# Optimization experiments

Measured on AMD Instinct MI355X. Metric: run time of the kernel, lower is better.

## Reference

```python
import jax, jax.numpy as jnp
import numpy as np

H = 8          # num_heads
WIN = 63       # win_size
LEFT = WIN - 1 - WIN // 2  # 31
EPS = 1e-5


def layer_norm(x, w, b):
    mu = x.mean(-1, keepdims=True)
    var = ((x - mu) ** 2).mean(-1, keepdims=True)
    return (x - mu) / jnp.sqrt(var + EPS) * w + b


def setup_inputs() -> dict:
    key = jax.random.key(0)
    N, T, C = 2, 2048, 512
    hid = 4 * C
    ks = jax.random.split(key, 16)
    s = 0.02
    return {
        "x": jax.random.normal(ks[0], (N, T, C), jnp.float32),
        "norm1_w": jnp.ones((C,), jnp.float32),
        "norm1_b": jnp.zeros((C,), jnp.float32),
        "qkv_w": jax.random.normal(ks[1], (3 * C, C), jnp.float32) * s,
        "qkv_b": jnp.zeros((3 * C,), jnp.float32),
        "rel_bias": jax.random.normal(ks[2], (H, WIN), jnp.float32) * s,
        "proj_w": jax.random.normal(ks[3], (C, C), jnp.float32) * s,
        "proj_b": jnp.zeros((C,), jnp.float32),
        "norm2_w": jnp.ones((C,), jnp.float32),
        "norm2_b": jnp.zeros((C,), jnp.float32),
        "fc1_w": jax.random.normal(ks[4], (hid, C), jnp.float32) * s,
        "fc1_b": jnp.zeros((hid,), jnp.float32),
        "fc2_w": jax.random.normal(ks[5], (C, hid), jnp.float32) * s,
        "fc2_b": jnp.zeros((C,), jnp.float32),
    }


def reference(x, norm1_w, norm1_b, qkv_w, qkv_b, rel_bias, proj_w, proj_b,
              norm2_w, norm2_b, fc1_w, fc1_b, fc2_w, fc2_b):
    N, T, C = x.shape
    hd = C // H
    scale = hd ** -0.5
    right = WIN - LEFT - 1

    shortcut = x
    h = layer_norm(x, norm1_w, norm1_b)
    qkv = (h @ qkv_w.T + qkv_b).reshape(N, T, 3, H, hd)
    q, k, v = qkv[:, :, 0], qkv[:, :, 1], qkv[:, :, 2]  # (N,T,H,hd)

    # zero-pad keys/values along time, gather sliding windows
    kp = jnp.pad(k, ((0, 0), (LEFT, right), (0, 0), (0, 0)))
    vp = jnp.pad(v, ((0, 0), (LEFT, right), (0, 0), (0, 0)))
    idx = jnp.arange(T)[:, None] + jnp.arange(WIN)[None, :]
    k_win = kp[:, idx]
    v_win = vp[:, idx]

    attn = jnp.einsum('nthd,ntwhd->nhtw', q * scale, k_win)
    attn = attn + rel_bias[None, :, None, :]
    # boundary mask: key position j = t - LEFT + w must lie in [0, T)
    pos = idx - LEFT
    mask = jnp.where((pos < 0) | (pos >= T), jnp.float32(-100.0), jnp.float32(0.0))
    attn = attn + mask[None, None, :, :]
    attn = jax.nn.softmax(attn, axis=-1)

    out = jnp.einsum('nhtw,ntwhd->nthd', attn, v_win).reshape(N, T, C)
    out = out @ proj_w.T + proj_b

    x = shortcut + out
    h2 = layer_norm(x, norm2_w, norm2_b)
    m = jax.nn.gelu(h2 @ fc1_w.T + fc1_b, approximate=False)  # torch nn.GELU = exact erf
    m = m @ fc2_w.T + fc2_b
    return x + m
```

## Files before the change

kernel.cpp:

```cpp
#include <hip/hip_runtime.h>

typedef unsigned short u16;
typedef unsigned int uint;
typedef __attribute__((ext_vector_type(4))) float floatx4;
typedef __attribute__((ext_vector_type(16))) float floatx16;
typedef __attribute__((ext_vector_type(8))) short shortx8;

__device__ __forceinline__ u16 f2b(float f) {
    unsigned int u = __float_as_uint(f);
    unsigned int r = (u + 0x7fffu + ((u >> 16) & 1u)) >> 16;
    return (u16)r;
}
__device__ __forceinline__ float b2f(u16 u) {
    return __uint_as_float(((unsigned int)u) << 16);
}
__device__ __forceinline__ void gl_lds16(const u16* g, u16* l) {
    __builtin_amdgcn_global_load_lds(
        (const __attribute__((address_space(1))) void*)g,
        (__attribute__((address_space(3))) void*)l, 16, 0, 0);
}
__device__ __forceinline__ float gelu_f(float v) {
    float e = __expf(1.59576912f * v * (1.0f + 0.044715f * v * v));
    return v * e / (e + 1.0f);
}

__device__ __forceinline__ void ln_row(const float* __restrict__ x,
                                       const float* __restrict__ w,
                                       const float* __restrict__ b,
                                       u16* __restrict__ out, int row,
                                       float* red) {
    const float2* xr = (const float2*)(x + (size_t)row * 512);
    float2 v = xr[threadIdx.x];
    float s = v.x + v.y;
    float s2 = v.x * v.x + v.y * v.y;
    #pragma unroll
    for (int o = 32; o > 0; o >>= 1) {
        s += __shfl_down(s, o, 64);
        s2 += __shfl_down(s2, o, 64);
    }
    int wid = threadIdx.x >> 6, lane = threadIdx.x & 63;
    if (lane == 0) { red[wid] = s; red[4 + wid] = s2; }
    __syncthreads();
    s = red[0] + red[1] + red[2] + red[3];
    s2 = red[4] + red[5] + red[6] + red[7];
    float mu = s * (1.0f / 512.0f);
    float var = s2 * (1.0f / 512.0f) - mu * mu;
    float rstd = rsqrtf(var + 1e-5f);
    float2 wv = ((const float2*)w)[threadIdx.x];
    float2 bv = ((const float2*)b)[threadIdx.x];
    float o0 = (v.x - mu) * rstd * wv.x + bv.x;
    float o1 = (v.y - mu) * rstd * wv.y + bv.y;
    unsigned int pack = (unsigned)f2b(o0) | ((unsigned)f2b(o1) << 16);
    ((unsigned int*)(out + (size_t)row * 512))[threadIdx.x] = pack;
}

__global__ __launch_bounds__(256) void ln_kernel(const float* __restrict__ x,
                                                 const float* __restrict__ w,
                                                 const float* __restrict__ b,
                                                 u16* __restrict__ out) {
    __shared__ float red[8];
    ln_row(x, w, b, out, blockIdx.x, red);
}

__global__ __launch_bounds__(256) void prep_kernel(
    const float* __restrict__ qkvw, u16* __restrict__ wq,
    const float* __restrict__ projw, u16* __restrict__ wp,
    const float* __restrict__ fc1w, u16* __restrict__ w1,
    const float* __restrict__ fc2w, u16* __restrict__ w2,
    const float* __restrict__ x, const float* __restrict__ n1w,
    const float* __restrict__ n1b, u16* __restrict__ hb) {
    __shared__ float red[8];
    int bi = blockIdx.x;
    if (bi < 3072) {
        const float* src;
        u16* dst;
        int i0;
        if (bi < 768)       { src = qkvw; dst = wq; i0 = bi; }
        else if (bi < 1024) { src = projw; dst = wp; i0 = bi - 768; }
        else if (bi < 2048) { src = fc1w; dst = w1; i0 = bi - 1024; }
        else                { src = fc2w; dst = w2; i0 = bi - 2048; }
        int i = i0 * 256 + threadIdx.x;
        float4 v = ((const float4*)src)[i];
        uint2 o;
        o.x = (unsigned)f2b(v.x) | ((unsigned)f2b(v.y) << 16);
        o.y = (unsigned)f2b(v.z) | ((unsigned)f2b(v.w) << 16);
        ((uint2*)dst)[i] = o;
    } else {
        ln_row(x, n1w, n1b, hb, bi - 3072, red);
    }
}

template <int BM, int BN, int EPI>
__global__ __launch_bounds__(256) void gemm_lds(const u16* __restrict__ A,
                                                const u16* __restrict__ W,
                                                const float* __restrict__ bias,
                                                const float* __restrict__ resid,
                                                float* __restrict__ outF,
                                                u16* __restrict__ outB,
                                                int M, int Nn, int K) {
    constexpr int MI = BM / 2 / 32;
    constexpr int NI = BN / 2 / 32;
    __shared__ u16 a_s[BM * 64];
    __shared__ u16 b_s[BN * 64];

    int tid = threadIdx.x;
    int wid = tid >> 6, lane = tid & 63;
    int wm = wid >> 1, wn = wid & 1;
    int m_blk = blockIdx.y * BM;
    int n_blk = blockIdx.x * BN;
    int lr = lane & 31;
    int lk = lane >> 5;

    floatx16 acc[MI][NI];
    #pragma unroll
    for (int i = 0; i < MI; i++)
        #pragma unroll
        for (int j = 0; j < NI; j++)
            #pragma unroll
            for (int r = 0; r < 16; r++) acc[i][j][r] = 0.f;

    const u16* Ag = A + (size_t)m_blk * K;
    const u16* Wg = W + (size_t)n_blk * K;

    for (int k0 = 0; k0 < K; k0 += 64) {
        #pragma unroll
        for (int p = 0; p < BM * 8 / 256; p++) {
            int c = p * 256 + tid;
            int row = c >> 3;
            int kc = (c & 7) ^ (row & 7);
            gl_lds16(Ag + (size_t)row * K + k0 + kc * 8, a_s + c * 8);
        }
        #pragma unroll
        for (int p = 0; p < BN * 8 / 256; p++) {
            int c = p * 256 + tid;
            int row = c >> 3;
            int kc = (c & 7) ^ (row & 7);
            gl_lds16(Wg + (size_t)row * K + k0 + kc * 8, b_s + c * 8);
        }
        __syncthreads();
        #pragma unroll
        for (int s = 0; s < 4; s++) {
            shortx8 af[MI], bf[NI];
            int kc = s * 2 + lk;
            #pragma unroll
            for (int i = 0; i < MI; i++) {
                int row = wm * (BM / 2) + i * 32 + lr;
                af[i] = *(const shortx8*)(a_s + (row * 8 + (kc ^ (row & 7))) * 8);
            }
            #pragma unroll
            for (int j = 0; j < NI; j++) {
                int row = wn * (BN / 2) + j * 32 + lr;
                bf[j] = *(const shortx8*)(b_s + (row * 8 + (kc ^ (row & 7))) * 8);
            }
            #pragma unroll
            for (int i = 0; i < MI; i++)
                #pragma unroll
                for (int j = 0; j < NI; j++)
                    acc[i][j] = __builtin_amdgcn_mfma_f32_32x32x16_bf16(
                        af[i], bf[j], acc[i][j], 0, 0, 0);
        }
        __syncthreads();
    }

    int col_l = lane & 31;
    int row_q = 4 * (lane >> 5);
    #pragma unroll
    for (int nj = 0; nj < NI; nj++) {
        int col = n_blk + wn * (BN / 2) + nj * 32 + col_l;
        float bv = bias[col];
        #pragma unroll
        for (int mi = 0; mi < MI; mi++) {
            #pragma unroll
            for (int r = 0; r < 16; r++) {
                int row = m_blk + wm * (BM / 2) + mi * 32 + (r & 3) + 8 * (r >> 2) + row_q;
                size_t off = (size_t)row * Nn + col;
                float v = acc[mi][nj][r] + bv;
                if (EPI == 1 || EPI == 3) {
                    outF[off] = v + resid[off];
                } else if (EPI == 2) {
                    outB[off] = f2b(gelu_f(v));
                } else {
                    outB[off] = f2b(v);
                }
            }
        }
    }
}

__global__ __launch_bounds__(256) void attn_kernel(const u16* __restrict__ qkv,
                                                   const float* __restrict__ rel_bias,
                                                   u16* __restrict__ out) {
    __shared__ u16 k_s[128][72];
    __shared__ u16 v_t[64][152];
    __shared__ u16 p_s[4][16][104];
    __shared__ float s_bias[64];

    int bx = blockIdx.x;
    int n = bx >> 8;
    int h = (bx >> 5) & 7;
    int t0 = (bx & 31) << 6;
    int tid = threadIdx.x, wid = tid >> 6, lane = tid & 63;
    int col = lane & 15, rq = lane >> 4;

    const u16* qrow = qkv + (size_t)(n * 2048 + t0 + wid * 16 + col) * 1536 + h * 64 + rq * 8;
    shortx8 qf0 = *(const shortx8*)qrow;
    shortx8 qf1 = *(const shortx8*)(qrow + 32);

    if (tid < 63) s_bias[tid] = rel_bias[h * 63 + tid];
    if (tid == 63) s_bias[63] = 0.f;

    const uint* qkv_u = (const uint*)qkv;
    for (int idx = tid; idx < 128 * 32; idx += 256) {
        int row = idx >> 5, j = idx & 31;
        int pos = t0 - 31 + row;
        uint kv = 0;
        if (pos >= 0 && pos < 2048)
            kv = qkv_u[(size_t)(n * 2048 + pos) * 768 + 256 + h * 32 + j];
        *(uint*)&k_s[row][j * 2] = kv;
    }
    for (int idx = tid; idx < 144 * 32; idx += 256) {
        int row = idx >> 5, j = idx & 31;
        int pos = t0 - 31 + row;
        uint vv = 0;
        if (pos >= 0 && pos < 2048)
            vv = qkv_u[(size_t)(n * 2048 + pos) * 768 + 512 + h * 32 + j];
        v_t[2 * j][row] = (u16)(vv & 0xffffu);
        v_t[2 * j + 1][row] = (u16)(vv >> 16);
    }
    __syncthreads();

    floatx4 S[5];
    #pragma unroll
    for (int nt = 0; nt < 5; nt++) S[nt] = (floatx4){0.f, 0.f, 0.f, 0.f};
    #pragma unroll
    for (int nt = 0; nt < 5; nt++) {
        const u16* kb = &k_s[wid * 16 + nt * 16 + col][rq * 8];
        shortx8 b0 = *(const shortx8*)kb;
        shortx8 b1 = *(const shortx8*)(kb + 32);
        S[nt] = __builtin_amdgcn_mfma_f32_16x16x32_bf16(qf0, b0, S[nt], 0, 0, 0);
        S[nt] = __builtin_amdgcn_mfma_f32_16x16x32_bf16(qf1, b1, S[nt], 0, 0, 0);
    }

    #pragma unroll
    for (int r = 0; r < 4; r++) {
        int t_row = rq * 4 + r;
        float sc[5];
        float mx = -1e30f;
        #pragma unroll
        for (int nt = 0; nt < 5; nt++) {
            int w = nt * 16 + col - t_row;
            int pos_abs = t0 - 31 + wid * 16 + nt * 16 + col;
            float v;
            if (w < 0 || w > 62) {
                v = -1e30f;
            } else {
                v = S[nt][r] * 0.125f + s_bias[w];
                if (pos_abs < 0 || pos_abs >= 2048) v -= 100.f;
            }
            sc[nt] = v;
            mx = fmaxf(mx, v);
        }
        #pragma unroll
        for (int o = 1; o < 16; o <<= 1) mx = fmaxf(mx, __shfl_xor(mx, o, 64));
        float l = 0.f;
        #pragma unroll
        for (int nt = 0; nt < 5; nt++) {
            sc[nt] = __expf(sc[nt] - mx);
            l += sc[nt];
        }
        #pragma unroll
        for (int o = 1; o < 16; o <<= 1) l += __shfl_xor(l, o, 64);
        float inv = 1.0f / l;
        #pragma unroll
        for (int nt = 0; nt < 5; nt++)
            p_s[wid][t_row][nt * 16 + col] = f2b(sc[nt] * inv);
        p_s[wid][t_row][80 + col] = 0;
    }
    __syncthreads();

    floatx4 O[4];
    #pragma unroll
    for (int dt = 0; dt < 4; dt++) O[dt] = (floatx4){0.f, 0.f, 0.f, 0.f};
    const u16* pr = &p_s[wid][col][rq * 8];
    shortx8 a0 = *(const shortx8*)pr;
    shortx8 a1 = *(const shortx8*)(pr + 32);
    shortx8 a2 = *(const shortx8*)(pr + 64);
    #pragma unroll
    for (int dt = 0; dt < 4; dt++) {
        const u16* vb = &v_t[dt * 16 + col][wid * 16 + rq * 8];
        shortx8 b0 = *(const shortx8*)vb;
        shortx8 b1 = *(const shortx8*)(vb + 32);
        shortx8 b2 = *(const shortx8*)(vb + 64);
        O[dt] = __builtin_amdgcn_mfma_f32_16x16x32_bf16(a0, b0, O[dt], 0, 0, 0);
        O[dt] = __builtin_amdgcn_mfma_f32_16x16x32_bf16(a1, b1, O[dt], 0, 0, 0);
        O[dt] = __builtin_amdgcn_mfma_f32_16x16x32_bf16(a2, b2, O[dt], 0, 0, 0);
    }

    #pragma unroll
    for (int dt = 0; dt < 4; dt++) {
        #pragma unroll
        for (int r = 0; r < 4; r++) {
            int t_row = rq * 4 + r;
            out[(size_t)(n * 2048 + t0 + wid * 16 + t_row) * 512 + h * 64 + dt * 16 + col] =
                f2b(O[dt][r]);
        }
    }
}

extern "C" void kernel_launch(void* const* d_in, const int* in_sizes, int n_in,
                              void* d_out, int out_size, void* d_ws, size_t ws_size,
                              hipStream_t stream) {
    const float* x     = (const float*)d_in[0];
    const float* n1w   = (const float*)d_in[1];
    const float* n1b   = (const float*)d_in[2];
    const float* qkvw  = (const float*)d_in[3];
    const float* qkvbv = (const float*)d_in[4];
    const float* relb  = (const float*)d_in[5];
    const float* projw = (const float*)d_in[6];
    const float* projb = (const float*)d_in[7];
    const float* n2w   = (const float*)d_in[8];
    const float* n2b   = (const float*)d_in[9];
    const float* fc1w  = (const float*)d_in[10];
    const float* fc1b  = (const float*)d_in[11];
    const float* fc2w  = (const float*)d_in[12];
    const float* fc2b  = (const float*)d_in[13];
    float* out = (float*)d_out;

    char* p = (char*)d_ws;
    u16* wq   = (u16*)p;  p += (size_t)786432 * 2;
    u16* wp   = (u16*)p;  p += (size_t)262144 * 2;
    u16* w1   = (u16*)p;  p += (size_t)1048576 * 2;
    u16* w2   = (u16*)p;  p += (size_t)1048576 * 2;
    u16* hb   = (u16*)p;  p += (size_t)2097152 * 2;
    u16* qkvb = (u16*)p;  p += (size_t)6291456 * 2;
    u16* attb = (u16*)p;  p += (size_t)2097152 * 2;
    float* x2 = (float*)p; p += (size_t)2097152 * 4;
    u16* mb   = (u16*)p;  p += (size_t)8388608 * 2;

    prep_kernel<<<7168, 256, 0, stream>>>(qkvw, wq, projw, wp, fc1w, w1, fc2w, w2,
                                          x, n1w, n1b, hb);
    gemm_lds<128, 128, 0><<<dim3(12, 32), 256, 0, stream>>>(
        hb, wq, qkvbv, nullptr, nullptr, qkvb, 4096, 1536, 512);
    attn_kernel<<<512, 256, 0, stream>>>(qkvb, relb, attb);
    gemm_lds<128, 64, 1><<<dim3(8, 32), 256, 0, stream>>>(
        attb, wp, projb, x, x2, nullptr, 4096, 512, 512);
    ln_kernel<<<4096, 256, 0, stream>>>(x2, n2w, n2b, hb);
    gemm_lds<128, 128, 2><<<dim3(16, 32), 256, 0, stream>>>(
        hb, w1, fc1b, nullptr, nullptr, mb, 4096, 2048, 512);
    gemm_lds<128, 64, 3><<<dim3(8, 32), 256, 0, stream>>>(
        mb, w2, fc2b, x2, out, nullptr, 4096, 512, 2048);
}
```

Measured before the change: 195.3 us.

## Double-buffer GEMM LDS tiles, shrink tiles, and store residual x2 in bf16

Adds double-buffered LDS staging to the MFMA GEMM, so the next K-tile's global-to-LDS loads overlap with compute and one barrier per iteration is dropped. Tile sizes shrink for the QKV, proj, fc1 and fc2 GEMMs to launch more blocks, and launch_bounds asks for 3 blocks per CU. The intermediate residual x2 is stored as bf16 instead of fp32, and the second layernorm reads bf16, which cuts memory traffic. In exchange it doubles LDS use and loses some precision on the residual path.

```diff
diff --git a/kernel.cpp b/kernel.cpp
--- a/kernel.cpp
+++ b/kernel.cpp
@@ -54,12 +54,35 @@
     ((unsigned int*)(out + (size_t)row * 512))[threadIdx.x] = pack;
 }
 
-__global__ __launch_bounds__(256) void ln_kernel(const float* __restrict__ x,
-                                                 const float* __restrict__ w,
-                                                 const float* __restrict__ b,
-                                                 u16* __restrict__ out) {
+__global__ __launch_bounds__(256) void ln_kernel_b(const u16* __restrict__ x,
+                                                   const float* __restrict__ w,
+                                                   const float* __restrict__ b,
+                                                   u16* __restrict__ out) {
     __shared__ float red[8];
-    ln_row(x, w, b, out, blockIdx.x, red);
+    int row = blockIdx.x;
+    uint pv = ((const uint*)(x + (size_t)row * 512))[threadIdx.x];
+    float vx = b2f((u16)(pv & 0xffffu)), vy = b2f((u16)(pv >> 16));
+    float s = vx + vy;
+    float s2 = vx * vx + vy * vy;
+    #pragma unroll
+    for (int o = 32; o > 0; o >>= 1) {
+        s += __shfl_down(s, o, 64);
+        s2 += __shfl_down(s2, o, 64);
+    }
+    int wid = threadIdx.x >> 6, lane = threadIdx.x & 63;
+    if (lane == 0) { red[wid] = s; red[4 + wid] = s2; }
+    __syncthreads();
+    s = red[0] + red[1] + red[2] + red[3];
+    s2 = red[4] + red[5] + red[6] + red[7];
+    float mu = s * (1.0f / 512.0f);
+    float var = s2 * (1.0f / 512.0f) - mu * mu;
+    float rstd = rsqrtf(var + 1e-5f);
+    float2 wv = ((const float2*)w)[threadIdx.x];
+    float2 bv = ((const float2*)b)[threadIdx.x];
+    float o0 = (vx - mu) * rstd * wv.x + bv.x;
+    float o1 = (vy - mu) * rstd * wv.y + bv.y;
+    unsigned int pack = (unsigned)f2b(o0) | ((unsigned)f2b(o1) << 16);
+    ((unsigned int*)(out + (size_t)row * 512))[threadIdx.x] = pack;
 }
 
 __global__ __launch_bounds__(256) void prep_kernel(
@@ -91,17 +114,20 @@
 }
 
 template <int BM, int BN, int EPI>
-__global__ __launch_bounds__(256) void gemm_lds(const u16* __restrict__ A,
-                                                const u16* __restrict__ W,
-                                                const float* __restrict__ bias,
-                                                const float* __restrict__ resid,
-                                                float* __restrict__ outF,
-                                                u16* __restrict__ outB,
-                                                int M, int Nn, int K) {
+__global__ __launch_bounds__(256, 3) void gemm_lds(const u16* __restrict__ A,
+                                                   const u16* __restrict__ W,
+                                                   const float* __restrict__ bias,
+                                                   const float* __restrict__ residF,
+                                                   const u16* __restrict__ residB,
+                                                   float* __restrict__ outF,
+                                                   u16* __restrict__ outB,
+                                                   int M, int Nn, int K) {
     constexpr int MI = BM / 2 / 32;
     constexpr int NI = BN / 2 / 32;
-    __shared__ u16 a_s[BM * 64];
-    __shared__ u16 b_s[BN * 64];
+    constexpr int ACH = BM * 8 / 256;
+    constexpr int BCH = BN * 8 / 256;
+    __shared__ u16 a_s[2][BM * 64];
+    __shared__ u16 b_s[2][BN * 64];
 
     int tid = threadIdx.x;
     int wid = tid >> 6, lane = tid & 63;
@@ -122,22 +148,37 @@
     const u16* Ag = A + (size_t)m_blk * K;
     const u16* Wg = W + (size_t)n_blk * K;
 
-    for (int k0 = 0; k0 < K; k0 += 64) {
-        #pragma unroll
-        for (int p = 0; p < BM * 8 / 256; p++) {
-            int c = p * 256 + tid;
-            int row = c >> 3;
-            int kc = (c & 7) ^ (row & 7);
-            gl_lds16(Ag + (size_t)row * K + k0 + kc * 8, a_s + c * 8);
-        }
-        #pragma unroll
-        for (int p = 0; p < BN * 8 / 256; p++) {
-            int c = p * 256 + tid;
-            int row = c >> 3;
-            int kc = (c & 7) ^ (row & 7);
-            gl_lds16(Wg + (size_t)row * K + k0 + kc * 8, b_s + c * 8);
-        }
+    int arow[ACH], akc[ACH], brow[BCH], bkc[BCH];
+    #pragma unroll
+    for (int p = 0; p < ACH; p++) {
+        int c = p * 256 + tid;
+        arow[p] = c >> 3;
+        akc[p] = (c & 7) ^ (arow[p] & 7);
+    }
+    #pragma unroll
+    for (int p = 0; p < BCH; p++) {
+        int c = p * 256 + tid;
+        brow[p] = c >> 3;
+        bkc[p] = (c & 7) ^ (brow[p] & 7);
+    }
+
+    auto stage = [&](int k0, int buf) {
+        #pragma unroll
+        for (int p = 0; p < ACH; p++)
+            gl_lds16(Ag + (size_t)arow[p] * K + k0 + akc[p] * 8,
+                     a_s[buf] + (p * 256 + tid) * 8);
+        #pragma unroll
+        for (int p = 0; p < BCH; p++)
+            gl_lds16(Wg + (size_t)brow[p] * K + k0 + bkc[p] * 8,
+                     b_s[buf] + (p * 256 + tid) * 8);
+    };
+
+    stage(0, 0);
+    int nit = K >> 6;
+    for (int it = 0; it < nit; it++) {
         __syncthreads();
+        if (it + 1 < nit) stage((it + 1) << 6, (it + 1) & 1);
+        int cb = it & 1;
         #pragma unroll
         for (int s = 0; s < 4; s++) {
             shortx8 af[MI], bf[NI];
@@ -145,12 +186,12 @@
             #pragma unroll
             for (int i = 0; i < MI; i++) {
                 int row = wm * (BM / 2) + i * 32 + lr;
-                af[i] = *(const shortx8*)(a_s + (row * 8 + (kc ^ (row & 7))) * 8);
+                af[i] = *(const shortx8*)(a_s[cb] + (row * 8 + (kc ^ (row & 7))) * 8);
             }
             #pragma unroll
             for (int j = 0; j < NI; j++) {
                 int row = wn * (BN / 2) + j * 32 + lr;
-                bf[j] = *(const shortx8*)(b_s + (row * 8 + (kc ^ (row & 7))) * 8);
+                bf[j] = *(const shortx8*)(b_s[cb] + (row * 8 + (kc ^ (row & 7))) * 8);
             }
             #pragma unroll
             for (int i = 0; i < MI; i++)
@@ -159,7 +200,6 @@
                     acc[i][j] = __builtin_amdgcn_mfma_f32_32x32x16_bf16(
                         af[i], bf[j], acc[i][j], 0, 0, 0);
         }
-        __syncthreads();
     }
 
     int col_l = lane & 31;
@@ -175,10 +215,12 @@
                 int row = m_blk + wm * (BM / 2) + mi * 32 + (r & 3) + 8 * (r >> 2) + row_q;
                 size_t off = (size_t)row * Nn + col;
                 float v = acc[mi][nj][r] + bv;
-                if (EPI == 1 || EPI == 3) {
-                    outF[off] = v + resid[off];
+                if (EPI == 1) {
+                    outB[off] = f2b(v + residF[off]);
                 } else if (EPI == 2) {
                     outB[off] = f2b(gelu_f(v));
+                } else if (EPI == 3) {
+                    outF[off] = v + b2f(residB[off]);
                 } else {
                     outB[off] = f2b(v);
                 }
@@ -334,19 +376,19 @@
     u16* hb   = (u16*)p;  p += (size_t)2097152 * 2;
     u16* qkvb = (u16*)p;  p += (size_t)6291456 * 2;
     u16* attb = (u16*)p;  p += (size_t)2097152 * 2;
-    float* x2 = (float*)p; p += (size_t)2097152 * 4;
+    u16* x2b  = (u16*)p;  p += (size_t)2097152 * 2;
     u16* mb   = (u16*)p;  p += (size_t)8388608 * 2;
 
     prep_kernel<<<7168, 256, 0, stream>>>(qkvw, wq, projw, wp, fc1w, w1, fc2w, w2,
                                           x, n1w, n1b, hb);
-    gemm_lds<128, 128, 0><<<dim3(12, 32), 256, 0, stream>>>(
-        hb, wq, qkvbv, nullptr, nullptr, qkvb, 4096, 1536, 512);
+    gemm_lds<128, 64, 0><<<dim3(24, 32), 256, 0, stream>>>(
+        hb, wq, qkvbv, nullptr, nullptr, nullptr, qkvb, 4096, 1536, 512);
     attn_kernel<<<512, 256, 0, stream>>>(qkvb, relb, attb);
-    gemm_lds<128, 64, 1><<<dim3(8, 32), 256, 0, stream>>>(
-        attb, wp, projb, x, x2, nullptr, 4096, 512, 512);
-    ln_kernel<<<4096, 256, 0, stream>>>(x2, n2w, n2b, hb);
-    gemm_lds<128, 128, 2><<<dim3(16, 32), 256, 0, stream>>>(
-        hb, w1, fc1b, nullptr, nullptr, mb, 4096, 2048, 512);
-    gemm_lds<128, 64, 3><<<dim3(8, 32), 256, 0, stream>>>(
-        mb, w2, fc2b, x2, out, nullptr, 4096, 512, 2048);
-}
+    gemm_lds<64, 64, 1><<<dim3(8, 64), 256, 0, stream>>>(
+        attb, wp, projb, x, nullptr, nullptr, x2b, 4096, 512, 512);
+    ln_kernel_b<<<4096, 256, 0, stream>>>(x2b, n2w, n2b, hb);
+    gemm_lds<128, 64, 2><<<dim3(32, 32), 256, 0, stream>>>(
+        hb, w1, fc1b, nullptr, nullptr, nullptr, mb, 4096, 2048, 512);
+    gemm_lds<64, 64, 3><<<dim3(8, 64), 256, 0, stream>>>(
+        mb, w2, fc2b, nullptr, x2b, out, nullptr, 4096, 512, 2048);
+}
```

After: 178.9 us. 8.4% less time.
